# Optimization experiments

Hardware: AMD Instinct MI355X
Metric: run time of the kernel (lower is better)

## Reference

```python
import jax, jax.numpy as jnp
import numpy as np

N, D, C, E, K = 100000, 64, 40, 1600000, 2

def setup_inputs() -> dict:
    key = jax.random.key(0)
    k1, k2, k3 = jax.random.split(key, 3)
    x = jax.random.normal(k1, (N, D), dtype=jnp.float32)
    edge_index = jax.random.randint(k2, (2, E), 0, N, dtype=jnp.int64)
    W = jax.random.normal(k3, (D, C), dtype=jnp.float32) * 0.05
    b = jnp.zeros((C,), dtype=jnp.float32)
    return {"x": x, "edge_index": edge_index, "W": W, "b": b}

def reference(x, edge_index, W, b):
    n = x.shape[0]
    self_loop = jnp.arange(n, dtype=edge_index.dtype)
    row = jnp.concatenate([edge_index[0], self_loop])  # [E+N]
    col = jnp.concatenate([edge_index[1], self_loop])  # [E+N]
    # degree over row (out-degree incl. self loops), as in torch_geometric.utils.degree
    deg = jax.ops.segment_sum(jnp.ones_like(row, dtype=x.dtype), row, num_segments=n)
    deg_inv_sqrt = jnp.where(deg > 0, jax.lax.rsqrt(deg), 0.0)
    norm = deg_inv_sqrt[row] * deg_inv_sqrt[col]  # [E+N]
    # K hops of SpMM: out[r] += norm_e * x[c] for each edge e=(r,c)
    for _ in range(K):
        x = jax.ops.segment_sum(norm[:, None] * x[col], row, num_segments=n)
    logits = x @ W + b  # [N, C]
    return jax.nn.log_softmax(logits, axis=1)
```

## Files before the change

### kernel.cpp

```cpp
#include <hip/hip_runtime.h>
#include <math.h>


#define D_FEAT 64
#define NCLS 40
#define NDW 20
#define NV4 5
#define BROWS 512
#define BROWS_LOG 9
#define BINCAP 10240
#define CSRCAP 12288
#define EPT 25

typedef float v2f __attribute__((ext_vector_type(2)));

__device__ __forceinline__ unsigned pack_bf16_2(float lo, float hi) {
    unsigned ulo = __float_as_uint(lo);
    unsigned uhi = __float_as_uint(hi);
    ulo = (ulo + 0x7fffu + ((ulo >> 16) & 1u)) >> 16;
    uhi = (uhi + 0x7fffu + ((uhi >> 16) & 1u)) & 0xffff0000u;
    return uhi | ulo;
}

__device__ __forceinline__ void acc2p(unsigned u, v2f& a) {
    v2f v;
    v.x = __uint_as_float(u << 16);
    v.y = __uint_as_float(u & 0xffff0000u);
    a += v;
}

__global__ __launch_bounds__(256) void bin_edges_kernel(const int* __restrict__ rows,
                                                        const int* __restrict__ cols,
                                                        int* __restrict__ bucket_cursor,
                                                        unsigned* __restrict__ bins,
                                                        int e, int nb) {
    __shared__ int cnt[512];
    for (int i = threadIdx.x; i < nb; i += 256) cnt[i] = 0;
    __syncthreads();
    int base = blockIdx.x * (256 * EPT) + threadIdx.x;
    int rr[EPT], cc[EPT];
#pragma unroll
    for (int k = 0; k < EPT; k++) {
        int idx = base + k * 256;
        if (idx < e) { rr[k] = rows[idx]; cc[k] = cols[idx]; }
        else { rr[k] = -1; cc[k] = 0; }
    }
#pragma unroll
    for (int k = 0; k < EPT; k++)
        if (rr[k] >= 0) atomicAdd(&cnt[rr[k] >> BROWS_LOG], 1);
    __syncthreads();
    for (int i = threadIdx.x; i < nb; i += 256) {
        int c = cnt[i];
        cnt[i] = (c > 0) ? atomicAdd(&bucket_cursor[i], c) : 0;
    }
    __syncthreads();
#pragma unroll
    for (int k = 0; k < EPT; k++) {
        if (rr[k] >= 0) {
            int b = rr[k] >> BROWS_LOG;
            int pos = atomicAdd(&cnt[b], 1);
            bins[(size_t)b * BINCAP + pos] =
                ((unsigned)(rr[k] & (BROWS - 1)) << 17) | (unsigned)cc[k];
        }
    }
}

__global__ __launch_bounds__(512) void build_csr_kernel(const unsigned* __restrict__ bins,
                                                        const int* __restrict__ bucket_cursor,
                                                        int* __restrict__ csr_col,
                                                        uint2* __restrict__ row_info,
                                                        float* __restrict__ dis,
                                                        uint4* __restrict__ pinfo, int n) {
    __shared__ int cnt[512];
    __shared__ int sm[512];
    __shared__ int cur[512];
    __shared__ int lcsr[CSRCAP];
    int b = blockIdx.x;
    int tid = threadIdx.x;
    int m = bucket_cursor[b];
    cnt[tid] = 0;
    __syncthreads();
    const unsigned* bp = bins + (size_t)b * BINCAP;
    for (int i = tid; i < m; i += 512) atomicAdd(&cnt[bp[i] >> 17], 1);
    __syncthreads();
    int c = cnt[tid];
    int padded = (c + 3) & ~3;
    int r = b * BROWS + tid;
    float dv = rsqrtf(1.0f + (float)c);
    if (r < n) dis[r] = dv;
    sm[tid] = padded;
    __syncthreads();
    for (int off = 1; off < 512; off <<= 1) {
        int t = (tid >= off) ? sm[tid - off] : 0;
        __syncthreads();
        sm[tid] += t;
        __syncthreads();
    }
    int off0 = sm[tid] - padded;
    cur[tid] = off0;
    if (r < n) row_info[r] = make_uint2((unsigned)(b * CSRCAP + off0), (unsigned)padded);
    __syncthreads();
    for (int i = tid; i < m; i += 512) {
        unsigned u = bp[i];
        int pos = atomicAdd(&cur[u >> 17], 1);
        lcsr[pos] = (int)(u & 0x1FFFFu);
    }
    __syncthreads();
    if (r < n) {
        for (int j = c; j < padded; j++) lcsr[off0 + j] = n;
    }
    __syncthreads();
    int tot = sm[511];
    int4* cp4 = (int4*)(csr_col + (size_t)b * CSRCAP);
    const int4* l4 = (const int4*)lcsr;
    for (int i = tid; i < (tot >> 2); i += 512) cp4[i] = l4[i];
    {
        int g = tot + tid;
        if (g < CSRCAP) csr_col[(size_t)b * CSRCAP + g] = n;
    }

    __syncthreads();
    if (tid < 64) cnt[tid] = 0;
    __syncthreads();
    int bin = min(padded >> 2, 63);
    if (r < n) atomicAdd(&cnt[bin], 1);
    __syncthreads();
    if (tid < 64) sm[tid] = cnt[tid];
    __syncthreads();
    for (int off = 1; off < 64; off <<= 1) {
        int t = (tid >= off && tid < 64) ? sm[tid - off] : 0;
        __syncthreads();
        if (tid < 64) sm[tid] += t;
        __syncthreads();
    }
    if (tid < 64) cur[tid] = sm[tid] - cnt[tid];
    __syncthreads();
    if (r < n) {
        int rank = atomicAdd(&cur[bin], 1);
        pinfo[b * BROWS + rank] = make_uint4((unsigned)(b * CSRCAP + off0),
                                             (unsigned)padded, (unsigned)r,
                                             __float_as_uint(dv));
    } else {
        pinfo[b * BROWS + tid] = make_uint4(0u, 0u, 0xFFFFFFFFu, 0u);
    }
}

__global__ __launch_bounds__(256) void sort_rows_kernel(int* __restrict__ csr_col,
                                                        const uint2* __restrict__ row_info,
                                                        int n) {
    int wid = (int)((blockIdx.x * blockDim.x + threadIdx.x) >> 6);
    int lane = threadIdx.x & 63;
    int r0 = wid * 2, r1 = r0 + 1;
    if (r0 >= n) return;
    uint2 i0 = row_info[r0];
    uint2 i1 = (r1 < n) ? row_info[r1] : make_uint2(0u, 0u);
    int p0 = (int)i0.y, p1 = (int)i1.y;
    if (p0 <= 32 && p1 <= 32) {
        int half = lane >> 5, hl = lane & 31;
        int base = half ? (int)i1.x : (int)i0.x;
        int pad  = half ? p1 : p0;
        int key = (hl < pad) ? csr_col[base + hl] : 0x7fffffff;
#pragma unroll
        for (int k = 2; k <= 32; k <<= 1) {
#pragma unroll
            for (int j = k >> 1; j > 0; j >>= 1) {
                int other = __shfl_xor(key, j, 64);
                bool takeMin = (((hl & j) == 0) == ((hl & k) == 0));
                int mn = min(key, other), mx = max(key, other);
                key = takeMin ? mn : mx;
            }
        }
        if (hl < pad) csr_col[base + hl] = key;
    } else {
        for (int t = 0; t < 2; t++) {
            int base = t ? (int)i1.x : (int)i0.x;
            int pad  = t ? p1 : p0;
            if (pad == 0) continue;
            if (pad <= 64) {
                int key = (lane < pad) ? csr_col[base + lane] : 0x7fffffff;
#pragma unroll
                for (int k = 2; k <= 64; k <<= 1) {
#pragma unroll
                    for (int j = k >> 1; j > 0; j >>= 1) {
                        int other = __shfl_xor(key, j, 64);
                        bool takeMin = (((lane & j) == 0) == ((lane & k) == 0));
                        int mn = min(key, other), mx = max(key, other);
                        key = takeMin ? mn : mx;
                    }
                }
                if (lane < pad) csr_col[base + lane] = key;
            } else if (lane == 0) {
                for (int i2 = 1; i2 < pad; i2++) {
                    int kk = csr_col[base + i2];
                    int j2 = i2 - 1;
                    while (j2 >= 0 && csr_col[base + j2] > kk) {
                        csr_col[base + j2 + 1] = csr_col[base + j2]; j2--;
                    }
                    csr_col[base + j2 + 1] = kk;
                }
            }
        }
    }
}

__global__ __launch_bounds__(256, 4) void xw_kernel(const float* __restrict__ x,
                                                    const float* __restrict__ W,
                                                    const float* __restrict__ dis,
                                                    unsigned* __restrict__ y0, int n) {
    __shared__ float Wl[D_FEAT][NCLS + 4];
    int t = threadIdx.x;
    for (int i = t; i < D_FEAT * NCLS; i += 256) {
        int d = i / NCLS, c = i - d * NCLS;
        Wl[d][c] = W[i];
    }
    __syncthreads();

    int wave = (blockIdx.x * 256 + t) >> 6;
    int lane = t & 63;
    int r0 = wave * 128 + lane;
    int r1 = r0 + 64;
    bool v0 = r0 < n, v1 = r1 < n;

    float acc0[NCLS], acc1[NCLS];
#pragma unroll
    for (int c = 0; c < NCLS; c++) { acc0[c] = 0.f; acc1[c] = 0.f; }

    const float4* xp0 = (const float4*)(x + (size_t)(v0 ? r0 : 0) * D_FEAT);
    const float4* xp1 = (const float4*)(x + (size_t)(v1 ? r1 : 0) * D_FEAT);
    for (int dg = 0; dg < 16; dg++) {
        float4 xa = xp0[dg];
        float4 xb = xp1[dg];
#pragma unroll
        for (int j = 0; j < 4; j++) {
            float a0 = (j == 0) ? xa.x : (j == 1) ? xa.y : (j == 2) ? xa.z : xa.w;
            float a1 = (j == 0) ? xb.x : (j == 1) ? xb.y : (j == 2) ? xb.z : xb.w;
            int d = dg * 4 + j;
#pragma unroll
            for (int c4 = 0; c4 < 10; c4++) {
                float4 wv = *(const float4*)&Wl[d][c4 * 4];
                acc0[c4 * 4 + 0] += a0 * wv.x; acc1[c4 * 4 + 0] += a1 * wv.x;
                acc0[c4 * 4 + 1] += a0 * wv.y; acc1[c4 * 4 + 1] += a1 * wv.y;
                acc0[c4 * 4 + 2] += a0 * wv.z; acc1[c4 * 4 + 2] += a1 * wv.z;
                acc0[c4 * 4 + 3] += a0 * wv.w; acc1[c4 * 4 + 3] += a1 * wv.w;
            }
        }
    }

    if (v0) {
        float s = dis[r0];
        unsigned* p = y0 + (size_t)r0 * NDW;
#pragma unroll
        for (int j = 0; j < NDW; j++)
            p[j] = pack_bf16_2(s * acc0[2 * j], s * acc0[2 * j + 1]);
    }
    if (v1) {
        float s = dis[r1];
        unsigned* p = y0 + (size_t)r1 * NDW;
#pragma unroll
        for (int j = 0; j < NDW; j++)
            p[j] = pack_bf16_2(s * acc1[2 * j], s * acc1[2 * j + 1]);
    }
}

#define ACCA(u) acc2p(u.x, h0A); acc2p(u.y, h1A); acc2p(u.z, h2A); acc2p(u.w, h3A);
#define ACCB(u) acc2p(u.x, h0B); acc2p(u.y, h1B); acc2p(u.z, h2B); acc2p(u.w, h3B);
#define GATHER8(cp, xs4, gl, base, len)                                     \
    uint4 cv0 = cp[(base >> 2)], cv1 = cp[(base >> 2) + 1];                 \
    uint4 u0 = xs4[cv0.x * NV4 + gl], u1 = xs4[cv0.y * NV4 + gl];           \
    uint4 u2 = xs4[cv0.z * NV4 + gl], u3 = xs4[cv0.w * NV4 + gl];           \
    uint4 u4 = xs4[cv1.x * NV4 + gl], u5 = xs4[cv1.y * NV4 + gl];           \
    uint4 u6 = xs4[cv1.z * NV4 + gl], u7 = xs4[cv1.w * NV4 + gl];           \
    __builtin_amdgcn_sched_barrier(0);                                      \
    if (base < len)     { ACCA(u0) ACCA(u1) ACCA(u2) ACCA(u3) }             \
    if (base + 4 < len) { ACCB(u4) ACCB(u5) ACCB(u6) ACCB(u7) }

__global__ __launch_bounds__(256, 5) void spmm_hop1_kernel(const uint4* __restrict__ xs_in,
                                                           uint4* __restrict__ xs_out,
                                                           const uint4* __restrict__ pinfo,
                                                           const int* __restrict__ csr_col,
                                                           int n, int nperm) {
    int wave = (blockIdx.x * blockDim.x + threadIdx.x) >> 6;
    int lane = threadIdx.x & 63;
    int e = lane / 5;
    int gl = lane - e * 5;
    int pidx = wave * 12 + e;
    bool inb = (e < 12) && (pidx < nperm);
    uint4 info = pinfo[inb ? pidx : 0];
    int s = (int)info.x;
    int len = inb ? (int)info.y : 0;
    int r = inb ? (int)info.z : -1;
    float dr = __uint_as_float(inb ? info.w : 0u);
    int maxlen = len;
#pragma unroll
    for (int o = 1; o < 64; o <<= 1) maxlen = max(maxlen, __shfl_xor(maxlen, o, 64));

    v2f h0A = {0.f,0.f}, h1A = {0.f,0.f}, h2A = {0.f,0.f}, h3A = {0.f,0.f};
    v2f h0B = {0.f,0.f}, h1B = {0.f,0.f}, h2B = {0.f,0.f}, h3B = {0.f,0.f};
    const uint4* cp = (const uint4*)(csr_col + s);
    for (int base = 0; base < maxlen; base += 8) {
        GATHER8(cp, xs_in, gl, base, len)
    }
    if (r >= 0 && r < n) {
        v2f h0 = h0A + h0B, h1 = h1A + h1B, h2 = h2A + h2B, h3 = h3A + h3B;
        uint4 us = xs_in[r * NV4 + gl];
        acc2p(us.x, h0); acc2p(us.y, h1); acc2p(us.z, h2); acc2p(us.w, h3);
        float d2 = dr * dr;
        uint4 o;
        o.x = pack_bf16_2(d2 * h0.x, d2 * h0.y);
        o.y = pack_bf16_2(d2 * h1.x, d2 * h1.y);
        o.z = pack_bf16_2(d2 * h2.x, d2 * h2.y);
        o.w = pack_bf16_2(d2 * h3.x, d2 * h3.y);
        xs_out[r * NV4 + gl] = o;
    }
}

__global__ __launch_bounds__(256, 5) void spmm_logits_kernel(const uint4* __restrict__ xs_in,
                                                             const uint4* __restrict__ pinfo,
                                                             const int* __restrict__ csr_col,
                                                             const float* __restrict__ b,
                                                             float* __restrict__ out,
                                                             int n, int nperm) {
    int wave = (blockIdx.x * blockDim.x + threadIdx.x) >> 6;
    int lane = threadIdx.x & 63;
    int e = lane / 5;
    int gl = lane - e * 5;
    int pidx = wave * 12 + e;
    bool inb = (e < 12) && (pidx < nperm);
    uint4 info = pinfo[inb ? pidx : 0];
    int s = (int)info.x;
    int len = inb ? (int)info.y : 0;
    int r = inb ? (int)info.z : -1;
    float dr = __uint_as_float(inb ? info.w : 0u);
    int maxlen = len;
#pragma unroll
    for (int o = 1; o < 64; o <<= 1) maxlen = max(maxlen, __shfl_xor(maxlen, o, 64));

    v2f h0A = {0.f,0.f}, h1A = {0.f,0.f}, h2A = {0.f,0.f}, h3A = {0.f,0.f};
    v2f h0B = {0.f,0.f}, h1B = {0.f,0.f}, h2B = {0.f,0.f}, h3B = {0.f,0.f};
    const uint4* cp = (const uint4*)(csr_col + s);
    for (int base = 0; base < maxlen; base += 8) {
        GATHER8(cp, xs_in, gl, base, len)
    }
    v2f h0 = h0A + h0B, h1 = h1A + h1B, h2 = h2A + h2B, h3 = h3A + h3B;
    uint4 us = (r >= 0 && r < n) ? xs_in[r * NV4 + gl] : make_uint4(0u, 0u, 0u, 0u);
    acc2p(us.x, h0); acc2p(us.y, h1); acc2p(us.z, h2); acc2p(us.w, h3);

    const float4* b4 = (const float4*)b;
    float4 ba = b4[gl * 2], bb = b4[gl * 2 + 1];
    float y0 = dr * h0.x + ba.x, y1 = dr * h0.y + ba.y;
    float y2 = dr * h1.x + ba.z, y3 = dr * h1.y + ba.w;
    float y4 = dr * h2.x + bb.x, y5 = dr * h2.y + bb.y;
    float y6 = dr * h3.x + bb.z, y7 = dr * h3.y + bb.w;

    int gb = ((e < 12) ? e : 11) * 5;
    float mloc = fmaxf(fmaxf(fmaxf(y0, y1), fmaxf(y2, y3)),
                       fmaxf(fmaxf(y4, y5), fmaxf(y6, y7)));
    float M = mloc;
#pragma unroll
    for (int k = 0; k < 5; k++) M = fmaxf(M, __shfl(mloc, gb + k, 64));
    float sloc = __expf(y0 - M) + __expf(y1 - M) + __expf(y2 - M) + __expf(y3 - M) +
                 __expf(y4 - M) + __expf(y5 - M) + __expf(y6 - M) + __expf(y7 - M);
    float S = 0.f;
#pragma unroll
    for (int k = 0; k < 5; k++) S += __shfl(sloc, gb + k, 64);
    float lse = M + __logf(S);

    if (r >= 0 && r < n) {
        float4* op = (float4*)(out + (size_t)r * NCLS) + gl * 2;
        op[0] = make_float4(y0 - lse, y1 - lse, y2 - lse, y3 - lse);
        op[1] = make_float4(y4 - lse, y5 - lse, y6 - lse, y7 - lse);
    }
}

extern "C" void kernel_launch(void* const* d_in, const int* in_sizes, int n_in,
                              void* d_out, int out_size, void* d_ws, size_t ws_size,
                              hipStream_t stream) {
    const float* x  = (const float*)d_in[0];
    const int*   ei = (const int*)d_in[1];
    const float* W  = (const float*)d_in[2];
    const float* b  = (const float*)d_in[3];
    float* out = (float*)d_out;

    const int n = in_sizes[0] / D_FEAT;
    const int e = in_sizes[1] / 2;
    const int nb = (n + BROWS - 1) / BROWS;

    const int* rows = ei;
    const int* cols = ei + e;

    size_t na = ((size_t)n + 256) & ~(size_t)255;
    size_t npm = (size_t)nb * BROWS;
    int*      bucket_cursor = (int*)d_ws;
    float*    dis           = (float*)(bucket_cursor + 256);
    uint2*    row_info      = (uint2*)(dis + na);
    uint4*    pinfo         = (uint4*)(row_info + na);
    unsigned* bins          = (unsigned*)(pinfo + npm);
    int*      csr_col       = (int*)(bins + (size_t)nb * BINCAP);
    unsigned* y0            = (unsigned*)(csr_col + (size_t)nb * CSRCAP);
    unsigned* y1            = y0 + (size_t)(n + 1) * NDW;

    const int BS = 256;

    hipMemsetAsync(bucket_cursor, 0, (size_t)nb * sizeof(int), stream);
    hipMemsetAsync(y0, 0, (size_t)(n + 1) * NDW * sizeof(unsigned) * 2, stream);
    {
        int blocks = (e + BS * EPT - 1) / (BS * EPT);
        bin_edges_kernel<<<blocks, BS, 0, stream>>>(rows, cols, bucket_cursor, bins, e, nb);
    }
    build_csr_kernel<<<nb, 512, 0, stream>>>(bins, bucket_cursor, csr_col, row_info, dis,
                                             pinfo, n);
    {
        int nwv = (n + 1) / 2;
        int sortBlocks = (nwv * 64 + BS - 1) / BS;
        sort_rows_kernel<<<sortBlocks, BS, 0, stream>>>(csr_col, row_info, n);
    }
    {
        int nwv = (n + 127) / 128;
        int blocks = (nwv + 3) / 4;
        xw_kernel<<<blocks, BS, 0, stream>>>(x, W, dis, y0, n);
    }

    int nperm = (int)npm;
    int nwaves = (nperm + 11) / 12;
    int blocks = (nwaves + 3) / 4;
    spmm_hop1_kernel<<<blocks, BS, 0, stream>>>((const uint4*)y0, (uint4*)y1, pinfo,
                                                csr_col, n, nperm);
    spmm_logits_kernel<<<blocks, BS, 0, stream>>>((const uint4*)y1, pinfo, csr_col,
                                                  b, out, n, nperm);
}
```

Baseline: 240.2 us.

## Replace memsets with tiny init kernel and simplify xw kernel to one row per thread

```diff
diff --git a/kernel.cpp b/kernel.cpp
--- a/kernel.cpp
+++ b/kernel.cpp
@@ -27,6 +27,17 @@
     v.x = __uint_as_float(u << 16);
     v.y = __uint_as_float(u & 0xffff0000u);
     a += v;
+}
+
+__global__ void init_kernel(int* __restrict__ bucket_cursor,
+                            unsigned* __restrict__ y0, unsigned* __restrict__ y1,
+                            int n, int nb) {
+    int i = threadIdx.x;
+    if (i < nb) bucket_cursor[i] = 0;
+    if (i < NDW) {
+        y0[(size_t)n * NDW + i] = 0u;
+        y1[(size_t)n * NDW + i] = 0u;
+    }
 }
 
 __global__ __launch_bounds__(256) void bin_edges_kernel(const int* __restrict__ rows,
@@ -203,62 +214,43 @@
     }
 }
 
-__global__ __launch_bounds__(256, 4) void xw_kernel(const float* __restrict__ x,
-                                                    const float* __restrict__ W,
-                                                    const float* __restrict__ dis,
-                                                    unsigned* __restrict__ y0, int n) {
-    __shared__ float Wl[D_FEAT][NCLS + 4];
-    int t = threadIdx.x;
-    for (int i = t; i < D_FEAT * NCLS; i += 256) {
-        int d = i / NCLS, c = i - d * NCLS;
-        Wl[d][c] = W[i];
-    }
-    __syncthreads();
-
-    int wave = (blockIdx.x * 256 + t) >> 6;
-    int lane = t & 63;
-    int r0 = wave * 128 + lane;
-    int r1 = r0 + 64;
-    bool v0 = r0 < n, v1 = r1 < n;
-
-    float acc0[NCLS], acc1[NCLS];
-#pragma unroll
-    for (int c = 0; c < NCLS; c++) { acc0[c] = 0.f; acc1[c] = 0.f; }
-
-    const float4* xp0 = (const float4*)(x + (size_t)(v0 ? r0 : 0) * D_FEAT);
-    const float4* xp1 = (const float4*)(x + (size_t)(v1 ? r1 : 0) * D_FEAT);
+__global__ __launch_bounds__(256) void xw_kernel(const float* __restrict__ x,
+                                                 const float* __restrict__ W,
+                                                 const float* __restrict__ dis,
+                                                 unsigned* __restrict__ y0, int n) {
+    int r = blockIdx.x * 256 + threadIdx.x;
+    if (r >= n) return;
+    float acc[NCLS];
+#pragma unroll
+    for (int c = 0; c < NCLS; c++) acc[c] = 0.f;
+    const float4* xp = (const float4*)(x + (size_t)r * D_FEAT);
+#pragma unroll 4
     for (int dg = 0; dg < 16; dg++) {
-        float4 xa = xp0[dg];
-        float4 xb = xp1[dg];
+        float4 xa = xp[dg];
 #pragma unroll
         for (int j = 0; j < 4; j++) {
-            float a0 = (j == 0) ? xa.x : (j == 1) ? xa.y : (j == 2) ? xa.z : xa.w;
-            float a1 = (j == 0) ? xb.x : (j == 1) ? xb.y : (j == 2) ? xb.z : xb.w;
+            float a = (j == 0) ? xa.x : (j == 1) ? xa.y : (j == 2) ? xa.z : xa.w;
             int d = dg * 4 + j;
 #pragma unroll
             for (int c4 = 0; c4 < 10; c4++) {
-                float4 wv = *(const float4*)&Wl[d][c4 * 4];
-                acc0[c4 * 4 + 0] += a0 * wv.x; acc1[c4 * 4 + 0] += a1 * wv.x;
-                acc0[c4 * 4 + 1] += a0 * wv.y; acc1[c4 * 4 + 1] += a1 * wv.y;
-                acc0[c4 * 4 + 2] += a0 * wv.z; acc1[c4 * 4 + 2] += a1 * wv.z;
-                acc0[c4 * 4 + 3] += a0 * wv.w; acc1[c4 * 4 + 3] += a1 * wv.w;
+                float4 wv = *(const float4*)(W + d * NCLS + c4 * 4);
+                acc[c4 * 4 + 0] += a * wv.x;
+                acc[c4 * 4 + 1] += a * wv.y;
+                acc[c4 * 4 + 2] += a * wv.z;
+                acc[c4 * 4 + 3] += a * wv.w;
             }
         }
     }
-
-    if (v0) {
-        float s = dis[r0];
-        unsigned* p = y0 + (size_t)r0 * NDW;
-#pragma unroll
-        for (int j = 0; j < NDW; j++)
-            p[j] = pack_bf16_2(s * acc0[2 * j], s * acc0[2 * j + 1]);
-    }
-    if (v1) {
-        float s = dis[r1];
-        unsigned* p = y0 + (size_t)r1 * NDW;
-#pragma unroll
-        for (int j = 0; j < NDW; j++)
-            p[j] = pack_bf16_2(s * acc1[2 * j], s * acc1[2 * j + 1]);
+    float s = dis[r];
+    uint4* p = (uint4*)(y0 + (size_t)r * NDW);
+#pragma unroll
+    for (int q = 0; q < NV4; q++) {
+        uint4 o;
+        o.x = pack_bf16_2(s * acc[8 * q + 0], s * acc[8 * q + 1]);
+        o.y = pack_bf16_2(s * acc[8 * q + 2], s * acc[8 * q + 3]);
+        o.z = pack_bf16_2(s * acc[8 * q + 4], s * acc[8 * q + 5]);
+        o.w = pack_bf16_2(s * acc[8 * q + 6], s * acc[8 * q + 7]);
+        p[q] = o;
     }
 }
 
@@ -401,8 +393,7 @@
 
     const int BS = 256;
 
-    hipMemsetAsync(bucket_cursor, 0, (size_t)nb * sizeof(int), stream);
-    hipMemsetAsync(y0, 0, (size_t)(n + 1) * NDW * sizeof(unsigned) * 2, stream);
+    init_kernel<<<1, 256, 0, stream>>>(bucket_cursor, y0, y1, n, nb);
     {
         int blocks = (e + BS * EPT - 1) / (BS * EPT);
         bin_edges_kernel<<<blocks, BS, 0, stream>>>(rows, cols, bucket_cursor, bins, e, nb);
@@ -415,8 +406,7 @@
         sort_rows_kernel<<<sortBlocks, BS, 0, stream>>>(csr_col, row_info, n);
     }
     {
-        int nwv = (n + 127) / 128;
-        int blocks = (nwv + 3) / 4;
+        int blocks = (n + BS - 1) / BS;
         xw_kernel<<<blocks, BS, 0, stream>>>(x, W, dis, y0, n);
     }
 
```

Measured after the change: 222.5 us. 7.4% less time.
